# Optimization experiments

Measured on AMD Instinct MI355X. Metric: run time of the kernel, lower is better.

The kernel has to match this reference:

```python
import jax, jax.numpy as jnp
import numpy as np

NUM_HEADS = 16
EPS = 1e-12  # F.normalize default eps


def _l2norm(x):
    # F.normalize(x, dim=-1): x / max(||x||_2, eps)
    n = jnp.sqrt(jnp.sum(x * x, axis=-1, keepdims=True))
    return x / jnp.maximum(n, EPS)


def setup_inputs() -> dict:
    key = jax.random.key(0)
    k1, k2, k3 = jax.random.split(key, 3)
    B, N, C = 16, 3136, 768
    x = jax.random.normal(k1, (B, N, C), dtype=jnp.float32)
    qkv_w = jax.random.normal(k2, (C, 3 * C), dtype=jnp.float32) * (1.0 / np.sqrt(C))
    temperature = jnp.ones((NUM_HEADS, 1, 1), dtype=jnp.float32)
    proj_w = jax.random.normal(k3, (C, C), dtype=jnp.float32) * (1.0 / np.sqrt(C))
    proj_b = jnp.zeros((C,), dtype=jnp.float32)
    return {"x": x, "qkv_w": qkv_w, "temperature": temperature,
            "proj_w": proj_w, "proj_b": proj_b}


def reference(x, qkv_w, temperature, proj_w, proj_b):
    B, N, C = x.shape
    H = NUM_HEADS
    D = C // H
    # qkv: [B,N,3C] -> [B,N,3,H,D] -> (3,B,H,D,N)
    qkv = (x @ qkv_w).reshape(B, N, 3, H, D).transpose(2, 0, 3, 4, 1)
    q, k, v = qkv[0], qkv[1], qkv[2]  # each [B,H,D,N]
    qn = _l2norm(q)  # normalize over token axis N
    kn = _l2norm(k)
    # cross-covariance: [B,H,D,D]
    attn = jnp.einsum('bhdn,bhen->bhde', qn, kn) * temperature
    attn = jax.nn.softmax(attn, axis=-1)
    out = jnp.einsum('bhde,bhen->bhdn', attn, v)  # [B,H,D,N]
    out = out.transpose(0, 3, 1, 2).reshape(B, N, C)
    return out @ proj_w + proj_b
```

## Files before the change

kernel.cpp:

```cpp
#include <hip/hip_runtime.h>

typedef unsigned short u16;
typedef unsigned int   u32;
typedef __attribute__((ext_vector_type(4))) float f32x4;
typedef __attribute__((ext_vector_type(8))) short bf16x8;
typedef __attribute__((ext_vector_type(8))) unsigned short u16x8;

#define MFMA16(a,b,c) __builtin_amdgcn_mfma_f32_16x16x32_bf16(a,b,c,0,0,0)

__device__ __forceinline__ u16 f32_bf16(float f){
  u32 u = __builtin_bit_cast(u32, f);
  u = (u + 0x7FFFu + ((u >> 16) & 1u)) >> 16;
  return (u16)u;
}

__device__ __forceinline__ void async_cp16(const u16* g, u16* l){
  __builtin_amdgcn_global_load_lds((const __attribute__((address_space(1))) u32*)g,
                                   (__attribute__((address_space(3))) u32*)l, 16, 0, 0);
}

__global__ __launch_bounds__(256)
void cvt_f32_bf16(const float* __restrict__ in, u16* __restrict__ out){
  size_t i = ((size_t)blockIdx.x * 256 + threadIdx.x) * 8;
  f32x4 a = *(const f32x4*)(in + i);
  f32x4 b = *(const f32x4*)(in + i + 4);
  u16x8 o;
  o[0]=f32_bf16(a[0]); o[1]=f32_bf16(a[1]); o[2]=f32_bf16(a[2]); o[3]=f32_bf16(a[3]);
  o[4]=f32_bf16(b[0]); o[5]=f32_bf16(b[1]); o[6]=f32_bf16(b[2]); o[7]=f32_bf16(b[3]);
  *(u16x8*)(out + i) = o;
}

__global__ __launch_bounds__(256)
void transpose_cvt(const float* __restrict__ w, u16* __restrict__ wt, int K, int N){
  __shared__ float tile[32][33];
  int n0 = blockIdx.x * 32, k0 = blockIdx.y * 32;
  int tx = threadIdx.x, ty = threadIdx.y;
#pragma unroll
  for (int j = 0; j < 32; j += 8) tile[ty + j][tx] = w[(size_t)(k0 + ty + j) * N + n0 + tx];
  __syncthreads();
#pragma unroll
  for (int j = 0; j < 32; j += 8)
    wt[(size_t)(n0 + ty + j) * K + k0 + tx] = f32_bf16(tile[tx][ty + j]);
}

template<int OUT_BF16, int BIAS>
__global__ __launch_bounds__(256)
void gemm_bt(const u16* __restrict__ A, const u16* __restrict__ Bt,
             void* __restrict__ Cv, const float* __restrict__ bias,
             int K, int lda, int ldc){
  __shared__ u16 sA[128 * 64];
  __shared__ u16 sB[128 * 64];
  const int tid  = threadIdx.x;
  const int lane = tid & 63;
  const int wave = tid >> 6;
  const int lrow = lane & 15, quad = lane >> 4;
  const int m0 = blockIdx.y * 128, n0 = blockIdx.x * 128;
  const int wm = (wave & 1) * 64, wn = (wave >> 1) * 64;
  const int sw = lrow & 7;
  const int col0 = ((0 * 4 + quad) ^ sw) * 8;
  const int col1 = ((1 * 4 + quad) ^ sw) * 8;

  f32x4 acc[4][4];
#pragma unroll
  for (int i = 0; i < 4; i++)
#pragma unroll
    for (int j = 0; j < 4; j++) acc[i][j] = (f32x4){0.f, 0.f, 0.f, 0.f};

  for (int kt = 0; kt < K; kt += 64){
#pragma unroll
    for (int i = 0; i < 4; i++){
      int c = i * 256 + tid;
      int m = c >> 3, kc = (c & 7) ^ (m & 7);
      async_cp16(A + (size_t)(m0 + m) * lda + kt + kc * 8, &sA[c * 8]);
    }
#pragma unroll
    for (int i = 0; i < 4; i++){
      int c = i * 256 + tid;
      int n = c >> 3, kc = (c & 7) ^ (n & 7);
      async_cp16(Bt + (size_t)(n0 + n) * K + kt + kc * 8, &sB[c * 8]);
    }
    __syncthreads();
#pragma unroll
    for (int kk = 0; kk < 2; kk++){
      const int col = kk ? col1 : col0;
      bf16x8 af[4], bfv[4];
#pragma unroll
      for (int mi = 0; mi < 4; mi++)
        af[mi] = *(const bf16x8*)&sA[(wm + mi * 16 + lrow) * 64 + col];
#pragma unroll
      for (int ni = 0; ni < 4; ni++)
        bfv[ni] = *(const bf16x8*)&sB[(wn + ni * 16 + lrow) * 64 + col];
#pragma unroll
      for (int mi = 0; mi < 4; mi++)
#pragma unroll
        for (int ni = 0; ni < 4; ni++)
          acc[mi][ni] = MFMA16(af[mi], bfv[ni], acc[mi][ni]);
    }
    __syncthreads();
  }
#pragma unroll
  for (int mi = 0; mi < 4; mi++){
#pragma unroll
    for (int ni = 0; ni < 4; ni++){
      int col = n0 + wn + ni * 16 + lrow;
      float bv = BIAS ? bias[col] : 0.f;
#pragma unroll
      for (int r = 0; r < 4; r++){
        int row = m0 + wm + mi * 16 + quad * 4 + r;
        float v = acc[mi][ni][r];
        if (OUT_BF16) ((u16*)Cv)[(size_t)row * ldc + col] = f32_bf16(v);
        else          ((float*)Cv)[(size_t)row * ldc + col] = v + bv;
      }
    }
  }
}

__global__ __launch_bounds__(256)
void attn_stats(const u16* __restrict__ qkvb, const float* __restrict__ temperature,
                u16* __restrict__ attnb){
  const int h = blockIdx.x, b = blockIdx.y;
  const int tid = threadIdx.x, wave = tid >> 6, lane = tid & 63;
  const int lrow = lane & 15, quad = lane >> 4;
  __shared__ struct {
    union {
      struct { u16 q[48 * 136]; u16 k[48 * 136]; } t;
      float red[2 * 15 * 256];
    } u;
    float S[48 * 49];
    float invq[48], invk[48];
  } sm;

  f32x4 acc[15];
#pragma unroll
  for (int t = 0; t < 15; t++) acc[t] = (f32x4){0.f, 0.f, 0.f, 0.f};

  const size_t rowbase = (size_t)b * 3136;
  const int cq = h * 48, ck = 768 + h * 48;

  for (int n0 = 0; n0 < 3136; n0 += 128){
    __syncthreads();
#pragma unroll
    for (int i = 0; i < 3; i++){
      int idx = i * 256 + tid;
      int n = idx / 6, dg = idx - n * 6;
      int gn = n0 + n;
      u16x8 vq, vk;
      if (gn < 3136){
        const u16* p = qkvb + (rowbase + gn) * 2304;
        vq = *(const u16x8*)(p + cq + dg * 8);
        vk = *(const u16x8*)(p + ck + dg * 8);
      } else {
        vq = (u16x8){0,0,0,0,0,0,0,0};
        vk = vq;
      }
#pragma unroll
      for (int j = 0; j < 8; j++){
        sm.u.t.q[(dg * 8 + j) * 136 + n] = vq[j];
        sm.u.t.k[(dg * 8 + j) * 136 + n] = vk[j];
      }
    }
    __syncthreads();
    bf16x8 qf[3], kf[3];
#pragma unroll
    for (int ti = 0; ti < 3; ti++){
      qf[ti] = *(const bf16x8*)&sm.u.t.q[(ti * 16 + lrow) * 136 + wave * 32 + quad * 8];
      kf[ti] = *(const bf16x8*)&sm.u.t.k[(ti * 16 + lrow) * 136 + wave * 32 + quad * 8];
    }
#pragma unroll
    for (int ti = 0; ti < 3; ti++)
#pragma unroll
      for (int tj = 0; tj < 3; tj++)
        acc[ti * 3 + tj] = MFMA16(qf[ti], kf[tj], acc[ti * 3 + tj]);
#pragma unroll
    for (int ti = 0; ti < 3; ti++){
      acc[9  + ti] = MFMA16(qf[ti], qf[ti], acc[9  + ti]);
      acc[12 + ti] = MFMA16(kf[ti], kf[ti], acc[12 + ti]);
    }
  }
  __syncthreads();
  if (wave < 2){
#pragma unroll
    for (int t = 0; t < 15; t++)
      *(f32x4*)&sm.u.red[(wave * 15 + t) * 256 + lane * 4] = acc[t];
  }
  __syncthreads();
  if (wave >= 2){
#pragma unroll
    for (int t = 0; t < 15; t++){
      f32x4* p = (f32x4*)&sm.u.red[((wave - 2) * 15 + t) * 256 + lane * 4];
      *p = *p + acc[t];
    }
  }
  __syncthreads();
  {
    const int p = tid;
    const int lr = p >> 2, rr = p & 3;
    const int row16 = ((lr >> 4) << 2) + rr, col16 = lr & 15;
#pragma unroll
    for (int t = 0; t < 9; t++){
      float v = sm.u.red[t * 256 + p] + sm.u.red[(15 + t) * 256 + p];
      sm.S[((t / 3) * 16 + row16) * 49 + (t % 3) * 16 + col16] = v;
    }
#pragma unroll
    for (int t = 9; t < 15; t++){
      float v = sm.u.red[t * 256 + p] + sm.u.red[(15 + t) * 256 + p];
      if (row16 == col16){
        if (t < 12) sm.invq[(t - 9)  * 16 + row16] = v;
        else        sm.invk[(t - 12) * 16 + row16] = v;
      }
    }
  }
  __syncthreads();
  if (tid < 96){
    float* arr = (tid < 48) ? sm.invq : sm.invk;
    int d = (tid < 48) ? tid : tid - 48;
    arr[d] = 1.0f / fmaxf(sqrtf(arr[d]), 1e-12f);
  }
  __syncthreads();
  if (tid < 48){
    const int d = tid;
    const float scale = sm.invq[d] * temperature[h];
    float lg[48];
    float mx = -1e30f;
#pragma unroll
    for (int e = 0; e < 48; e++){
      lg[e] = sm.S[d * 49 + e] * scale * sm.invk[e];
      mx = fmaxf(mx, lg[e]);
    }
    float s = 0.f;
#pragma unroll
    for (int e = 0; e < 48; e++){ float ex = __expf(lg[e] - mx); lg[e] = ex; s += ex; }
    const float inv = 1.f / s;
    u16* dst = attnb + ((size_t)(b * 16 + h) * 48 + d) * 64;
#pragma unroll
    for (int e = 0; e < 48; e++) dst[e] = f32_bf16(lg[e] * inv);
#pragma unroll
    for (int e = 48; e < 64; e++) dst[e] = 0;
  }
}

__global__ __launch_bounds__(256)
void attn_apply_v(const u16* __restrict__ qkvb, const u16* __restrict__ attnb,
                  u16* __restrict__ outm){
  const int h = blockIdx.y, b = blockIdx.z;
  const int nb = blockIdx.x * 256;
  const int tid = threadIdx.x, wave = tid >> 6, lane = tid & 63;
  const int lrow = lane & 15, quad = lane >> 4;
  __shared__ u16 sA[48 * 72];
#pragma unroll
  for (int i = 0; i < 2; i++){
    int idx = i * 256 + tid;
    if (idx < 384){
      int d = idx >> 3, eg = idx & 7;
      *(u16x8*)&sA[d * 72 + eg * 8] =
        *(const u16x8*)&attnb[((size_t)(b * 16 + h) * 48 + d) * 64 + eg * 8];
    }
  }
  __syncthreads();
  bf16x8 bfr[3][2];
#pragma unroll
  for (int tj = 0; tj < 3; tj++){
    bfr[tj][0] = *(const bf16x8*)&sA[(tj * 16 + lrow) * 72 + quad * 8];
    bfr[tj][1] = *(const bf16x8*)&sA[(tj * 16 + lrow) * 72 + 32 + quad * 8];
  }
  f32x4 acc[4][3];
#pragma unroll
  for (int i = 0; i < 4; i++)
#pragma unroll
    for (int j = 0; j < 3; j++) acc[i][j] = (f32x4){0.f, 0.f, 0.f, 0.f};

  const size_t vbase = (size_t)b * 3136 * 2304 + 1536 + h * 48;
  const int eo1 = 32 + ((quad < 2) ? quad * 8 : 0);
#pragma unroll
  for (int mi = 0; mi < 4; mi++){
    int n = nb + wave * 64 + mi * 16 + lrow;
    int nc = n < 3136 ? n : 3135;
    const u16* vp = qkvb + vbase + (size_t)nc * 2304;
    bf16x8 a0 = *(const bf16x8*)(vp + quad * 8);
    bf16x8 a1 = *(const bf16x8*)(vp + eo1);
#pragma unroll
    for (int tj = 0; tj < 3; tj++){
      acc[mi][tj] = MFMA16(a0, bfr[tj][0], acc[mi][tj]);
      acc[mi][tj] = MFMA16(a1, bfr[tj][1], acc[mi][tj]);
    }
  }
#pragma unroll
  for (int mi = 0; mi < 4; mi++)
#pragma unroll
    for (int tj = 0; tj < 3; tj++){
      int col = h * 48 + tj * 16 + lrow;
#pragma unroll
      for (int r = 0; r < 4; r++){
        int n = nb + wave * 64 + mi * 16 + quad * 4 + r;
        if (n < 3136)
          outm[((size_t)b * 3136 + n) * 2304 + col] = f32_bf16(acc[mi][tj][r]);
      }
    }
}

extern "C" void kernel_launch(void* const* d_in, const int* in_sizes, int n_in,
                              void* d_out, int out_size, void* d_ws, size_t ws_size,
                              hipStream_t stream){
  const float* x      = (const float*)d_in[0];
  const float* qkv_w  = (const float*)d_in[1];
  const float* temp   = (const float*)d_in[2];
  const float* proj_w = (const float*)d_in[3];
  const float* proj_b = (const float*)d_in[4];
  float* out = (float*)d_out;
  char* ws = (char*)d_ws;

  const size_t OFF_XB   = 0;
  const size_t OFF_WQ   = 77070336;
  const size_t OFF_WP   = 80609280;
  const size_t OFF_QKV  = 81788928;
  const size_t OFF_ATTN = 312999936;

  u16* xb    = (u16*)(ws + OFF_XB);
  u16* wqt   = (u16*)(ws + OFF_WQ);
  u16* wpt   = (u16*)(ws + OFF_WP);
  u16* qkvb  = (u16*)(ws + OFF_QKV);
  u16* attnb = (u16*)(ws + OFF_ATTN);

  cvt_f32_bf16<<<dim3(18816), dim3(256), 0, stream>>>(x, xb);
  transpose_cvt<<<dim3(2304 / 32, 768 / 32), dim3(32, 8), 0, stream>>>(qkv_w, wqt, 768, 2304);
  transpose_cvt<<<dim3(768 / 32, 768 / 32), dim3(32, 8), 0, stream>>>(proj_w, wpt, 768, 768);
  gemm_bt<1, 0><<<dim3(18, 392), dim3(256), 0, stream>>>(xb, wqt, qkvb, nullptr, 768, 768, 2304);
  attn_stats<<<dim3(16, 16), dim3(256), 0, stream>>>(qkvb, temp, attnb);
  attn_apply_v<<<dim3(13, 16, 16), dim3(256), 0, stream>>>(qkvb, attnb, qkvb);
  gemm_bt<0, 1><<<dim3(6, 392), dim3(256), 0, stream>>>(qkvb, wpt, out, proj_b, 768, 2304, 768);
}
```

Before: 700.9 us.

## Store QKV in per-head contiguous panels to coalesce attention loads

The QKV GEMM now writes its output in a head-major panel layout of [which*16+head][B*N][48] rather than row-major [B*N][2304]. The attention kernels read these contiguous 48-wide rows, and attn_stats transposes into shared memory with paired 32-bit stores. The output projection GEMM gathers its A operand from the per-head panels. This is meant to cut strided global accesses and bank conflicts in the attention stages, at the cost of scattered 2-byte stores in the GEMM epilogue and div/mod address math in the gather.

```diff
diff --git a/kernel.cpp b/kernel.cpp
--- a/kernel.cpp
+++ b/kernel.cpp
@@ -7,6 +7,8 @@
 typedef __attribute__((ext_vector_type(8))) unsigned short u16x8;
 
 #define MFMA16(a,b,c) __builtin_amdgcn_mfma_f32_16x16x32_bf16(a,b,c,0,0,0)
+
+#define PANEL 2408448u
 
 __device__ __forceinline__ u16 f32_bf16(float f){
   u32 u = __builtin_bit_cast(u32, f);
@@ -43,7 +45,7 @@
     wt[(size_t)(n0 + ty + j) * K + k0 + tx] = f32_bf16(tile[tx][ty + j]);
 }
 
-template<int OUT_BF16, int BIAS>
+template<int OUT_BF16, int BIAS, int A_GATHER, int C_HEADS>
 __global__ __launch_bounds__(256)
 void gemm_bt(const u16* __restrict__ A, const u16* __restrict__ Bt,
              void* __restrict__ Cv, const float* __restrict__ bias,
@@ -71,7 +73,16 @@
     for (int i = 0; i < 4; i++){
       int c = i * 256 + tid;
       int m = c >> 3, kc = (c & 7) ^ (m & 7);
-      async_cp16(A + (size_t)(m0 + m) * lda + kt + kc * 8, &sA[c * 8]);
+      const u16* src;
+      if (A_GATHER){
+        unsigned k0 = (unsigned)(kt + kc * 8);
+        unsigned hh = k0 / 48u;
+        unsigned dd = k0 - hh * 48u;
+        src = A + (size_t)hh * PANEL + (size_t)(m0 + m) * 48 + dd;
+      } else {
+        src = A + (size_t)(m0 + m) * lda + kt + kc * 8;
+      }
+      async_cp16(src, &sA[c * 8]);
     }
 #pragma unroll
     for (int i = 0; i < 4; i++){
@@ -103,20 +114,33 @@
 #pragma unroll
     for (int ni = 0; ni < 4; ni++){
       int col = n0 + wn + ni * 16 + lrow;
-      float bv = BIAS ? bias[col] : 0.f;
-#pragma unroll
-      for (int r = 0; r < 4; r++){
-        int row = m0 + wm + mi * 16 + quad * 4 + r;
-        float v = acc[mi][ni][r];
-        if (OUT_BF16) ((u16*)Cv)[(size_t)row * ldc + col] = f32_bf16(v);
-        else          ((float*)Cv)[(size_t)row * ldc + col] = v + bv;
+      if (OUT_BF16 && C_HEADS){
+        unsigned which = (unsigned)col / 768u;
+        unsigned rem   = (unsigned)col - which * 768u;
+        unsigned hh    = rem / 48u;
+        unsigned dd    = rem - hh * 48u;
+        u16* cb = (u16*)Cv + (size_t)(which * 16u + hh) * PANEL + dd;
+#pragma unroll
+        for (int r = 0; r < 4; r++){
+          int row = m0 + wm + mi * 16 + quad * 4 + r;
+          cb[(size_t)row * 48] = f32_bf16(acc[mi][ni][r]);
+        }
+      } else {
+        float bv = BIAS ? bias[col] : 0.f;
+#pragma unroll
+        for (int r = 0; r < 4; r++){
+          int row = m0 + wm + mi * 16 + quad * 4 + r;
+          float v = acc[mi][ni][r];
+          if (OUT_BF16) ((u16*)Cv)[(size_t)row * ldc + col] = f32_bf16(v);
+          else          ((float*)Cv)[(size_t)row * ldc + col] = v + bv;
+        }
       }
     }
   }
 }
 
 __global__ __launch_bounds__(256)
-void attn_stats(const u16* __restrict__ qkvb, const float* __restrict__ temperature,
+void attn_stats(const u16* __restrict__ qkv2, const float* __restrict__ temperature,
                 u16* __restrict__ attnb){
   const int h = blockIdx.x, b = blockIdx.y;
   const int tid = threadIdx.x, wave = tid >> 6, lane = tid & 63;
@@ -134,30 +158,24 @@
 #pragma unroll
   for (int t = 0; t < 15; t++) acc[t] = (f32x4){0.f, 0.f, 0.f, 0.f};
 
-  const size_t rowbase = (size_t)b * 3136;
-  const int cq = h * 48, ck = 768 + h * 48;
+  const u16* qbase = qkv2 + (size_t)h        * PANEL + (size_t)b * 3136 * 48;
+  const u16* kbase = qkv2 + (size_t)(16 + h) * PANEL + (size_t)b * 3136 * 48;
 
   for (int n0 = 0; n0 < 3136; n0 += 128){
     __syncthreads();
 #pragma unroll
     for (int i = 0; i < 3; i++){
-      int idx = i * 256 + tid;
-      int n = idx / 6, dg = idx - n * 6;
-      int gn = n0 + n;
-      u16x8 vq, vk;
-      if (gn < 3136){
-        const u16* p = qkvb + (rowbase + gn) * 2304;
-        vq = *(const u16x8*)(p + cq + dg * 8);
-        vk = *(const u16x8*)(p + ck + dg * 8);
-      } else {
-        vq = (u16x8){0,0,0,0,0,0,0,0};
-        vk = vq;
-      }
-#pragma unroll
-      for (int j = 0; j < 8; j++){
-        sm.u.t.q[(dg * 8 + j) * 136 + n] = vq[j];
-        sm.u.t.k[(dg * 8 + j) * 136 + n] = vk[j];
-      }
+      int wgrp = i * 4 + wave;
+      int qk = wgrp >= 6;
+      int dg = qk ? wgrp - 6 : wgrp;
+      int n  = n0 + lane * 2;
+      const u16* src = (qk ? kbase : qbase) + (size_t)n * 48 + dg * 8;
+      u16x8 va = (n     < 3136) ? *(const u16x8*)src        : (u16x8){0,0,0,0,0,0,0,0};
+      u16x8 vb = (n + 1 < 3136) ? *(const u16x8*)(src + 48) : (u16x8){0,0,0,0,0,0,0,0};
+      u16* dst = qk ? sm.u.t.k : sm.u.t.q;
+#pragma unroll
+      for (int j = 0; j < 8; j++)
+        *(u32*)&dst[(dg * 8 + j) * 136 + lane * 2] = (u32)va[j] | ((u32)vb[j] << 16);
     }
     __syncthreads();
     bf16x8 qf[3], kf[3];
@@ -240,7 +258,7 @@
 }
 
 __global__ __launch_bounds__(256)
-void attn_apply_v(const u16* __restrict__ qkvb, const u16* __restrict__ attnb,
+void attn_apply_v(const u16* __restrict__ qkv2, const u16* __restrict__ attnb,
                   u16* __restrict__ outm){
   const int h = blockIdx.y, b = blockIdx.z;
   const int nb = blockIdx.x * 256;
@@ -269,13 +287,13 @@
 #pragma unroll
     for (int j = 0; j < 3; j++) acc[i][j] = (f32x4){0.f, 0.f, 0.f, 0.f};
 
-  const size_t vbase = (size_t)b * 3136 * 2304 + 1536 + h * 48;
+  const u16* vpanel = qkv2 + (size_t)(32 + h) * PANEL + (size_t)b * 3136 * 48;
   const int eo1 = 32 + ((quad < 2) ? quad * 8 : 0);
 #pragma unroll
   for (int mi = 0; mi < 4; mi++){
     int n = nb + wave * 64 + mi * 16 + lrow;
     int nc = n < 3136 ? n : 3135;
-    const u16* vp = qkvb + vbase + (size_t)nc * 2304;
+    const u16* vp = vpanel + (size_t)nc * 48;
     bf16x8 a0 = *(const bf16x8*)(vp + quad * 8);
     bf16x8 a1 = *(const bf16x8*)(vp + eo1);
 #pragma unroll
@@ -284,16 +302,16 @@
       acc[mi][tj] = MFMA16(a1, bfr[tj][1], acc[mi][tj]);
     }
   }
+  u16* opanel = outm + (size_t)h * PANEL + (size_t)b * 3136 * 48;
 #pragma unroll
   for (int mi = 0; mi < 4; mi++)
 #pragma unroll
     for (int tj = 0; tj < 3; tj++){
-      int col = h * 48 + tj * 16 + lrow;
+      int d = tj * 16 + lrow;
 #pragma unroll
       for (int r = 0; r < 4; r++){
         int n = nb + wave * 64 + mi * 16 + quad * 4 + r;
-        if (n < 3136)
-          outm[((size_t)b * 3136 + n) * 2304 + col] = f32_bf16(acc[mi][tj][r]);
+        if (n < 3136) opanel[(size_t)n * 48 + d] = f32_bf16(acc[mi][tj][r]);
       }
     }
 }
@@ -318,14 +336,14 @@
   u16* xb    = (u16*)(ws + OFF_XB);
   u16* wqt   = (u16*)(ws + OFF_WQ);
   u16* wpt   = (u16*)(ws + OFF_WP);
-  u16* qkvb  = (u16*)(ws + OFF_QKV);
+  u16* qkv2  = (u16*)(ws + OFF_QKV);
   u16* attnb = (u16*)(ws + OFF_ATTN);
 
   cvt_f32_bf16<<<dim3(18816), dim3(256), 0, stream>>>(x, xb);
   transpose_cvt<<<dim3(2304 / 32, 768 / 32), dim3(32, 8), 0, stream>>>(qkv_w, wqt, 768, 2304);
   transpose_cvt<<<dim3(768 / 32, 768 / 32), dim3(32, 8), 0, stream>>>(proj_w, wpt, 768, 768);
-  gemm_bt<1, 0><<<dim3(18, 392), dim3(256), 0, stream>>>(xb, wqt, qkvb, nullptr, 768, 768, 2304);
-  attn_stats<<<dim3(16, 16), dim3(256), 0, stream>>>(qkvb, temp, attnb);
-  attn_apply_v<<<dim3(13, 16, 16), dim3(256), 0, stream>>>(qkvb, attnb, qkvb);
-  gemm_bt<0, 1><<<dim3(6, 392), dim3(256), 0, stream>>>(qkvb, wpt, out, proj_b, 768, 2304, 768);
-}
+  gemm_bt<1, 0, 0, 1><<<dim3(18, 392), dim3(256), 0, stream>>>(xb, wqt, qkv2, nullptr, 768, 768, 0);
+  attn_stats<<<dim3(16, 16), dim3(256), 0, stream>>>(qkv2, temp, attnb);
+  attn_apply_v<<<dim3(13, 16, 16), dim3(256), 0, stream>>>(qkv2, attnb, qkv2);
+  gemm_bt<0, 1, 1, 0><<<dim3(6, 392), dim3(256), 0, stream>>>(qkv2, wpt, out, proj_b, 768, 0, 768);
+}
```

Measured after the change: 683.3 us. 1.03x faster.
